# Optimization experiments

Hardware: AMD Instinct MI355X
Metric: run time of the kernel (lower is better)

## Reference

```python
import jax, jax.numpy as jnp
import numpy as np

M, N, T = 4, 48, 512
D_IN = M + N                 # GRU-net input dim (m+n)
H1 = D_IN * 10 * 8           # 4160
HID = M * M + N * N          # 2320 GRU hidden
H2 = M * N * 4               # 768
D_OUT = M * N                # 192


def setup_inputs() -> dict:
    key = jax.random.key(0)
    ks = jax.random.split(key, 12)
    s = lambda i, shape, sc=0.02: (jax.random.normal(ks[i], shape, jnp.float32) * sc)
    return {
        "A": jnp.eye(M, dtype=jnp.float32) + s(0, (M, M), 0.05),
        "C": s(1, (N, M + 1), 0.1),
        "x0": jax.random.normal(ks[2], (M,), jnp.float32),
        "h0": jax.random.normal(ks[3], (HID,), jnp.float32),  # randn init hidden (zero_hidden_state=False)
        "y_seq": jax.random.normal(ks[4], (N, T), jnp.float32),
        "W1": s(5, (H1, D_IN)), "b1": jnp.zeros((H1,), jnp.float32),
        "W_ih": s(6, (3 * HID, H1)), "W_hh": s(7, (3 * HID, HID)),
        "b_ih": jnp.zeros((3 * HID,), jnp.float32), "b_hh": jnp.zeros((3 * HID,), jnp.float32),
        "W2": s(8, (H2, HID)), "b2": jnp.zeros((H2,), jnp.float32),
        "W3": s(9, (D_OUT, H2)), "b3": jnp.zeros((D_OUT,), jnp.float32),
    }


def _l2norm(v):
    # torch F.normalize(p=2, eps=1e-12): v / max(||v||, eps)
    return v / jnp.maximum(jnp.linalg.norm(v), 1e-12)


def _gru_cell(x, h, W_ih, W_hh, b_ih, b_hh):
    gi = W_ih @ x + b_ih
    gh = W_hh @ h + b_hh
    i_r, i_z, i_n = jnp.split(gi, 3)
    h_r, h_z, h_n = jnp.split(gh, 3)
    r = jax.nn.sigmoid(i_r + h_r)
    z = jax.nn.sigmoid(i_z + h_z)
    n = jnp.tanh(i_n + r * h_n)
    return (1.0 - z) * n + z * h


def reference(A, C, x0, h0, y_seq, W1, b1, W_ih, W_hh, b_ih, b_hh, W2, b2, W3, b3):
    one = jnp.ones((1,), jnp.float32)

    def step(carry, y):
        x_prior, x_post, h = carry
        # step_prior (linear case)
        x_prev_prior = x_prior
        x_prior = A @ x_post
        m1y = C @ jnp.concatenate([x_prior, one])  # [N]
        # step_KGain_est: KGainNet_in = [norm(dy), norm(dx)]
        knet_in = jnp.concatenate([_l2norm(y - m1y), _l2norm(x_post - x_prev_prior)])
        l1 = jax.nn.relu(W1 @ knet_in + b1)
        h = _gru_cell(l1, h, W_ih, W_hh, b_ih, b_hh)
        l2 = jax.nn.relu(W2 @ h + b2)
        kg = ((W3 @ l2 + b3) / 10000.0).reshape(M, N)
        # KNet_step posterior update
        x_post = x_prior + kg @ (y - m1y)
        return (x_prior, x_post, h), x_post

    _, xs = jax.lax.scan(step, (x0, x0, h0), y_seq.T)  # scan over T
    return xs.T  # [M, T], matches forward_sequence output
```

## Files before the change

### kernel.cpp

```cpp
#include <hip/hip_runtime.h>
#include <stdint.h>
#include <stddef.h>

typedef float v2f __attribute__((ext_vector_type(2)));

#define HID   2320
#define G3    6960
#define KIH   4160
#define KHH   2320
#define NBLK  232
#define NL2B  192
#define NTHR  512
#define UPB   10
#define TSEQ  512
#define KRES  1600
#define INVWS (1.0f/128.0f)
#define SPINCAP (1u<<17)

#define WS_WIH8 0L
#define WS_W1E  28953600L
#define WS_HBP  29219840L
#define WS_SLT  29279232L
#define WS_END  29308928L

struct Offs {
  int l1s, hs, wih, whh, w2s, w3s, cs, as_, b3s, bih, bhh, b2s, gis, ghs,
      ts, inn, kn, dxs, xpri, xpo, b4, nrm, l2r, slp;
  int total;
};

__host__ __device__ inline Offs mkoffs(int res) {
  Offs o; int p = 0;
#define ALLOC(name, bytes) { p = (p + 15) & ~15; o.name = p; p += (bytes); }
  ALLOC(l1s, KIH*4) ALLOC(hs, HID*4)
  ALLOC(wih, res ? 30*KRES : 16) ALLOC(whh, res ? 30*KHH : 16)
  ALLOC(w2s, res ? 4*HID : 16)
  ALLOC(w3s, 16*48*4) ALLOC(cs, 240*4) ALLOC(as_, 64) ALLOC(b3s, 192*4)
  ALLOC(bih, 120) ALLOC(bhh, 120) ALLOC(b2s, 16)
  ALLOC(gis, 120) ALLOC(ghs, 120)
  ALLOC(ts, 64) ALLOC(inn, 192) ALLOC(kn, 256)
  ALLOC(dxs, 16) ALLOC(xpri, 16) ALLOC(xpo, 16) ALLOC(b4, 16) ALLOC(nrm, 16)
  ALLOC(l2r, 16) ALLOC(slp, 64)
#undef ALLOC
  o.total = (p + 63) & ~63;
  return o;
}

struct Params {
  const float *A, *C, *x0, *h0, *y, *W1, *b1, *Wih, *Whh, *bih, *bhh, *W2, *b2, *W3, *b3;
  const uint8_t *wih8, *w1e;
  uint64_t *hbp, *slt;
  float *out;
  int resident;
};

__device__ __forceinline__ uint8_t f2fp8(float v) {
  v = fminf(fmaxf(v * 128.f, -448.f), 448.f);
  int pk = __builtin_amdgcn_cvt_pk_fp8_f32(v, v, 0, false);
  return (uint8_t)(pk & 0xff);
}

__device__ __forceinline__ void pub64(uint64_t* a, uint32_t tag, float v) {
  uint64_t w = ((uint64_t)tag << 32) | (uint64_t)__float_as_uint(v);
  __hip_atomic_store(a, w, __ATOMIC_RELAXED, __HIP_MEMORY_SCOPE_AGENT);
}

template<int N>
__device__ __forceinline__ void poll_pkt(const uint64_t* base, uint32_t want,
                                         float* out, bool& dead) {
  uint64_t v[N];
  uint32_t spins = 0;
  for (;;) {
    bool ok = true;
#pragma unroll
    for (int k = 0; k < N; ++k)
      v[k] = __hip_atomic_load(base + k, __ATOMIC_RELAXED, __HIP_MEMORY_SCOPE_AGENT);
#pragma unroll
    for (int k = 0; k < N; ++k) ok &= ((uint32_t)(v[k] >> 32) == want);
    if (ok || dead) break;
    ++spins;
    if (spins > 8) __builtin_amdgcn_s_sleep(2);
    if (spins > SPINCAP) dead = true;
  }
#pragma unroll
  for (int k = 0; k < N; ++k) out[k] = __uint_as_float((uint32_t)v[k]);
}

__device__ __forceinline__ void dot8_lds(
    const float* __restrict__ acts, const uint8_t* __restrict__ w, int stride,
    int K, const int* lrows, int nr, int lane, float acc[4])
{
  int kb = 0;
  for (; kb + 256 <= K; kb += 256) {
    const float4 a = ((const float4*)(acts + kb))[lane];
#pragma unroll
    for (int j = 0; j < 4; ++j) if (j < nr) {
      uint32_t wb = *(const uint32_t*)(w + (size_t)lrows[j]*stride + kb + (lane<<2));
      v2f lo = __builtin_amdgcn_cvt_pk_f32_fp8((int)wb, false);
      v2f hi = __builtin_amdgcn_cvt_pk_f32_fp8((int)wb, true);
      acc[j] = fmaf(lo.x, a.x, acc[j]); acc[j] = fmaf(lo.y, a.y, acc[j]);
      acc[j] = fmaf(hi.x, a.z, acc[j]); acc[j] = fmaf(hi.y, a.w, acc[j]);
    }
  }
  int rem = K - kb;
  if ((lane << 2) < rem) {
    const float4 a = ((const float4*)(acts + kb))[lane];
#pragma unroll
    for (int j = 0; j < 4; ++j) if (j < nr) {
      uint32_t wb = *(const uint32_t*)(w + (size_t)lrows[j]*stride + kb + (lane<<2));
      v2f lo = __builtin_amdgcn_cvt_pk_f32_fp8((int)wb, false);
      v2f hi = __builtin_amdgcn_cvt_pk_f32_fp8((int)wb, true);
      acc[j] = fmaf(lo.x, a.x, acc[j]); acc[j] = fmaf(lo.y, a.y, acc[j]);
      acc[j] = fmaf(hi.x, a.z, acc[j]); acc[j] = fmaf(hi.y, a.w, acc[j]);
    }
  }
}

__device__ __forceinline__ void dot8_glb(
    const float* __restrict__ acts, const uint8_t* __restrict__ gw, int gstride,
    int K0, int K, const int* grows, int nr, int lane, float acc[4])
{
  int kb = K0;
  for (; kb + 512 <= K; kb += 512) {
    const float4 a0 = ((const float4*)(acts + kb))[lane*2];
    const float4 a1 = ((const float4*)(acts + kb))[lane*2 + 1];
#pragma unroll
    for (int j = 0; j < 4; ++j) if (j < nr) {
      uint2 wb = *(const uint2*)(gw + (size_t)grows[j]*gstride + kb + (lane<<3));
      v2f l0 = __builtin_amdgcn_cvt_pk_f32_fp8((int)wb.x, false);
      v2f h0 = __builtin_amdgcn_cvt_pk_f32_fp8((int)wb.x, true);
      v2f l1 = __builtin_amdgcn_cvt_pk_f32_fp8((int)wb.y, false);
      v2f h1 = __builtin_amdgcn_cvt_pk_f32_fp8((int)wb.y, true);
      acc[j] = fmaf(l0.x, a0.x, acc[j]); acc[j] = fmaf(l0.y, a0.y, acc[j]);
      acc[j] = fmaf(h0.x, a0.z, acc[j]); acc[j] = fmaf(h0.y, a0.w, acc[j]);
      acc[j] = fmaf(l1.x, a1.x, acc[j]); acc[j] = fmaf(l1.y, a1.y, acc[j]);
      acc[j] = fmaf(h1.x, a1.z, acc[j]); acc[j] = fmaf(h1.y, a1.w, acc[j]);
    }
  }
  for (int e = kb + lane; e < K; e += 64) {
    float a = acts[e];
#pragma unroll
    for (int j = 0; j < 4; ++j) if (j < nr) {
      v2f lo = __builtin_amdgcn_cvt_pk_f32_fp8(
          (int)(uint32_t)gw[(size_t)grows[j]*gstride + e], false);
      acc[j] = fmaf(lo.x, a, acc[j]);
    }
  }
}

__device__ __forceinline__ void dotf_glb(
    const float* __restrict__ acts, const float* __restrict__ gw, int gstride,
    int K, const int* grows, int nr, int lane, float acc[4])
{
  for (int k = lane; k < K; k += 64) {
    float a = acts[k];
#pragma unroll
    for (int j = 0; j < 4; ++j) if (j < nr)
      acc[j] = fmaf(gw[(size_t)grows[j]*gstride + k], a, acc[j]);
  }
}

extern "C" __global__ void __launch_bounds__(NTHR, 2) knet_main(Params p)
{
  extern __shared__ char smem[];
  const Offs o = mkoffs(p.resident);
  float*   L1S  = (float*)(smem + o.l1s);
  float*   HS   = (float*)(smem + o.hs);
  uint8_t* WIHR = (uint8_t*)(smem + o.wih);
  uint8_t* WHHR = (uint8_t*)(smem + o.whh);
  uint8_t* W2S  = (uint8_t*)(smem + o.w2s);
  float*   W3S  = (float*)(smem + o.w3s);
  float*   CS   = (float*)(smem + o.cs);
  float*   AS   = (float*)(smem + o.as_);
  float*   B3S  = (float*)(smem + o.b3s);
  float*   BIH  = (float*)(smem + o.bih);
  float*   BHH  = (float*)(smem + o.bhh);
  float*   B2S  = (float*)(smem + o.b2s);
  float*   GIS  = (float*)(smem + o.gis);
  float*   GHS  = (float*)(smem + o.ghs);
  float*   TS   = (float*)(smem + o.ts);
  float*   INNS = (float*)(smem + o.inn);
  float*   KN   = (float*)(smem + o.kn);
  float*   DXS  = (float*)(smem + o.dxs);
  float*   XPRI = (float*)(smem + o.xpri);
  float*   XPO  = (float*)(smem + o.xpo);
  float*   B4   = (float*)(smem + o.b4);
  float*   NRM  = (float*)(smem + o.nrm);
  float*   L2R  = (float*)(smem + o.l2r);
  float*   SLP  = (float*)(smem + o.slp);

  const int tid  = (int)threadIdx.x;
  const int bid  = (int)blockIdx.x;
  const int lane = tid & 63;
  const int wv   = tid >> 6;
  const int rows2 = (bid < NL2B) ? 4 : 0;
  const int r2s   = bid * 4;
  bool dead = false;

  int lrows[4] = {0,0,0,0}, grows[4] = {0,0,0,0};
  int nr = 0;
#pragma unroll
  for (int j = 0; j < 4; ++j) {
    int row = wv + 8*j;
    if (row < 30) { int u = row/3, g = row - 3*u;
      lrows[nr] = row; grows[nr] = g*HID + bid*UPB + u; ++nr; }
  }

  for (int i = tid; i < rows2*192; i += NTHR) { int rl = i/192, rem = i - rl*192;
    W3S[i] = p.W3[(size_t)rem*768 + (r2s + rl)]; }
  for (int i = tid; i < 240; i += NTHR) CS[i] = p.C[i];
  if (tid < 16) AS[tid] = p.A[tid];
  for (int i = tid; i < 192; i += NTHR) B3S[i] = p.b3[i];
  if (tid < rows2) B2S[tid] = p.b2[r2s + tid];
  if (tid < 30) {
    int u = tid/3, g = tid - 3*u, ug = bid*UPB + u;
    BIH[tid] = p.bih[g*HID + ug];
    BHH[tid] = p.bhh[g*HID + ug];
  }
  for (int i = tid; i < HID; i += NTHR) HS[i] = p.h0[i];
  if (p.resident) {
    const int kd = KRES >> 2;
    uint32_t* W32 = (uint32_t*)WIHR;
    for (int i = tid; i < 30*kd; i += NTHR) {
      int row = i / kd, c = i - row*kd;
      int u = row/3, g = row - 3*u, gr = g*HID + bid*UPB + u;
      W32[i] = ((const uint32_t*)p.wih8)[(size_t)gr*(KIH/4) + c];
    }
    for (int i = tid; i < 30*KHH; i += NTHR) {
      int row = i / KHH, k = i - row*KHH;
      int u = row/3, g = row - 3*u, gr = g*HID + bid*UPB + u;
      WHHR[i] = f2fp8(p.Whh[(size_t)gr*KHH + k]);
    }
    for (int i = tid; i < rows2*HID; i += NTHR) {
      int rl = i / HID, k = i - rl*HID;
      W2S[i] = f2fp8(p.W2[(size_t)(r2s+rl)*HID + k]);
    }
  }
  uint2 pf[4][5];
#pragma unroll
  for (int j = 0; j < 4; ++j)
#pragma unroll
    for (int i = 0; i < 5; ++i) pf[j][i] = make_uint2(0u, 0u);
#pragma unroll
  for (int j = 0; j < 4; ++j) if (j < nr)
#pragma unroll
    for (int i = 0; i < 5; ++i)
      pf[j][i] = *(const uint2*)(p.wih8 + (size_t)grows[j]*KIH + KRES + i*512 + (lane<<3));
  __syncthreads();

  auto small_chain = [&](int ycol) {
    if (tid < 48) {
      float s = CS[tid*5 + 4];
#pragma unroll
      for (int k = 0; k < 4; ++k) s += CS[tid*5 + k] * XPRI[k];
      INNS[tid] = p.y[(size_t)tid*TSEQ + ycol] - s;
    }
    __syncthreads();
    if (wv == 0) {
      float q = (lane < 48) ? INNS[lane]*INNS[lane] : 0.f;
#pragma unroll
      for (int m = 32; m >= 1; m >>= 1) q += __shfl_xor(q, m, 64);
      if (lane == 0) NRM[0] = fmaxf(sqrtf(q), 1e-12f);
    } else if (wv == 1) {
      float q = (lane < 4) ? DXS[lane]*DXS[lane] : 0.f;
#pragma unroll
      for (int m = 32; m >= 1; m >>= 1) q += __shfl_xor(q, m, 64);
      if (lane == 0) NRM[1] = fmaxf(sqrtf(q), 1e-12f);
    }
    __syncthreads();
    if (tid < 48) KN[tid] = INNS[tid] / NRM[0];
    else if (tid < 52) KN[tid] = DXS[tid-48] / NRM[1];
    else if (tid == 52) KN[tid] = 1.0f;
    else if (tid < 64) KN[tid] = 0.0f;
    else if (tid < 68) {
      int i = tid - 64; float s = 0;
      for (int j = 0; j < 48; ++j) s += B3S[i*48 + j] * INNS[j];
      B4[i] = s;
    }
    if (tid >= 128 && tid < 128 + rows2*4) {
      int idx = tid - 128, rl = idx >> 2, i = idx & 3;
      float s = 0;
      for (int j = 0; j < 48; ++j) s += W3S[rl*192 + i*48 + j] * INNS[j];
      TS[i*4 + rl] = s;
    }
    __syncthreads();
    {
      float4 kn[16];
#pragma unroll
      for (int c = 0; c < 16; ++c) kn[c] = ((const float4*)KN)[c];
      for (int r = tid; r < KIH; r += NTHR) {
        const uint4* wp = (const uint4*)(p.w1e + (size_t)r*64);
        float acc = 0.f;
#pragma unroll
        for (int q = 0; q < 4; ++q) {
          uint4 w = wp[q];
          v2f l0 = __builtin_amdgcn_cvt_pk_f32_fp8((int)w.x, false);
          v2f h0 = __builtin_amdgcn_cvt_pk_f32_fp8((int)w.x, true);
          v2f l1 = __builtin_amdgcn_cvt_pk_f32_fp8((int)w.y, false);
          v2f h1 = __builtin_amdgcn_cvt_pk_f32_fp8((int)w.y, true);
          v2f l2 = __builtin_amdgcn_cvt_pk_f32_fp8((int)w.z, false);
          v2f h2 = __builtin_amdgcn_cvt_pk_f32_fp8((int)w.z, true);
          v2f l3 = __builtin_amdgcn_cvt_pk_f32_fp8((int)w.w, false);
          v2f h3 = __builtin_amdgcn_cvt_pk_f32_fp8((int)w.w, true);
          float4 a0 = kn[q*4+0], a1 = kn[q*4+1], a2 = kn[q*4+2], a3 = kn[q*4+3];
          acc = fmaf(l0.x,a0.x,acc); acc = fmaf(l0.y,a0.y,acc);
          acc = fmaf(h0.x,a0.z,acc); acc = fmaf(h0.y,a0.w,acc);
          acc = fmaf(l1.x,a1.x,acc); acc = fmaf(l1.y,a1.y,acc);
          acc = fmaf(h1.x,a1.z,acc); acc = fmaf(h1.y,a1.w,acc);
          acc = fmaf(l2.x,a2.x,acc); acc = fmaf(l2.y,a2.y,acc);
          acc = fmaf(h2.x,a2.z,acc); acc = fmaf(h2.y,a2.w,acc);
          acc = fmaf(l3.x,a3.x,acc); acc = fmaf(l3.y,a3.y,acc);
          acc = fmaf(h3.x,a3.z,acc); acc = fmaf(h3.y,a3.w,acc);
        }
        L1S[r] = fmaxf(acc * INVWS, 0.f);
      }
    }
    __syncthreads();
  };

  auto ghh = [&]() {
    float acc[4] = {0,0,0,0};
    if (p.resident) dot8_lds(HS, WHHR, KHH, KHH, lrows, nr, lane, acc);
    else            dotf_glb(HS, p.Whh, KHH, KHH, grows, nr, lane, acc);
#pragma unroll
    for (int m = 32; m >= 1; m >>= 1)
#pragma unroll
      for (int j = 0; j < 4; ++j) acc[j] += __shfl_xor(acc[j], m, 64);
    if (lane == 0)
#pragma unroll
      for (int j = 0; j < 4; ++j) if (j < nr) GHS[lrows[j]] = acc[j];
  };

  if (tid < 4) { XPO[tid] = p.x0[tid]; DXS[tid] = 0.f; }
  __syncthreads();
  if (tid < 4) {
    float s = 0;
#pragma unroll
    for (int j = 0; j < 4; ++j) s += AS[tid*4 + j] * XPO[j];
    XPRI[tid] = s;
  }
  __syncthreads();
  small_chain(0);
  ghh();
  __syncthreads();

  for (int t = 0; t < TSEQ; ++t) {
    const int par = t & 1;
    const uint32_t want = (uint32_t)(t + 1);

    {
      float acc[4] = {0,0,0,0};
      if (p.resident) dot8_lds(L1S, WIHR, KRES, KRES, lrows, nr, lane, acc);
      else            dot8_glb(L1S, p.wih8, KIH, 0, KRES, grows, nr, lane, acc);
#pragma unroll
      for (int i = 0; i < 5; ++i) {
        const float4 a0 = ((const float4*)(L1S + KRES + i*512))[lane*2];
        const float4 a1 = ((const float4*)(L1S + KRES + i*512))[lane*2 + 1];
#pragma unroll
        for (int j = 0; j < 4; ++j) if (j < nr) {
          uint2 w = pf[j][i];
          v2f l0 = __builtin_amdgcn_cvt_pk_f32_fp8((int)w.x, false);
          v2f h0 = __builtin_amdgcn_cvt_pk_f32_fp8((int)w.x, true);
          v2f l1v = __builtin_amdgcn_cvt_pk_f32_fp8((int)w.y, false);
          v2f h1 = __builtin_amdgcn_cvt_pk_f32_fp8((int)w.y, true);
          acc[j] = fmaf(l0.x, a0.x, acc[j]); acc[j] = fmaf(l0.y, a0.y, acc[j]);
          acc[j] = fmaf(h0.x, a0.z, acc[j]); acc[j] = fmaf(h0.y, a0.w, acc[j]);
          acc[j] = fmaf(l1v.x, a1.x, acc[j]); acc[j] = fmaf(l1v.y, a1.y, acc[j]);
          acc[j] = fmaf(h1.x, a1.z, acc[j]); acc[j] = fmaf(h1.y, a1.w, acc[j]);
        }
      }
#pragma unroll
      for (int m = 32; m >= 1; m >>= 1)
#pragma unroll
        for (int j = 0; j < 4; ++j) acc[j] += __shfl_xor(acc[j], m, 64);
      if (lane == 0)
#pragma unroll
        for (int j = 0; j < 4; ++j) if (j < nr) GIS[lrows[j]] = acc[j];
    }
    __syncthreads();

    if (tid < UPB) {
      int ug = bid*UPB + tid, r0 = tid*3;
      float gi0 = GIS[r0+0]*INVWS + BIH[r0+0], gh0 = GHS[r0+0]*INVWS + BHH[r0+0];
      float gi1 = GIS[r0+1]*INVWS + BIH[r0+1], gh1 = GHS[r0+1]*INVWS + BHH[r0+1];
      float gi2 = GIS[r0+2]*INVWS + BIH[r0+2], gh2 = GHS[r0+2]*INVWS + BHH[r0+2];
      float rg = 1.f/(1.f + expf(-(gi0+gh0)));
      float zg = 1.f/(1.f + expf(-(gi1+gh1)));
      float ng = tanhf(gi2 + rg*gh2);
      float hnew = (1.f - zg)*ng + zg*HS[ug];
      pub64(p.hbp + (((size_t)par*NBLK + bid) << 4) + tid, want, hnew);
    }
    __syncthreads();

    if (wv < 4) {
      int idx = (wv << 6) | lane;
      if (idx < NBLK) {
        float v[10];
        poll_pkt<10>(p.hbp + (((size_t)par*NBLK + idx) << 4), want, v, dead);
#pragma unroll
        for (int k = 0; k < 10; ++k) HS[idx*10 + k] = v[k];
      }
    }
    __syncthreads();

    if (rows2 && wv >= 4) {
      const int rl = wv - 4;
      float a2 = 0.f;
      if (p.resident) {
        int kb = 0;
        for (; kb + 256 <= HID; kb += 256) {
          const float4 a = ((const float4*)(HS + kb))[lane];
          uint32_t wb = *(const uint32_t*)(W2S + rl*HID + kb + (lane<<2));
          v2f lo = __builtin_amdgcn_cvt_pk_f32_fp8((int)wb, false);
          v2f hi = __builtin_amdgcn_cvt_pk_f32_fp8((int)wb, true);
          a2 = fmaf(lo.x, a.x, a2); a2 = fmaf(lo.y, a.y, a2);
          a2 = fmaf(hi.x, a.z, a2); a2 = fmaf(hi.y, a.w, a2);
        }
        if ((lane << 2) < HID - kb) {
          const float4 a = ((const float4*)(HS + kb))[lane];
          uint32_t wb = *(const uint32_t*)(W2S + rl*HID + kb + (lane<<2));
          v2f lo = __builtin_amdgcn_cvt_pk_f32_fp8((int)wb, false);
          v2f hi = __builtin_amdgcn_cvt_pk_f32_fp8((int)wb, true);
          a2 = fmaf(lo.x, a.x, a2); a2 = fmaf(lo.y, a.y, a2);
          a2 = fmaf(hi.x, a.z, a2); a2 = fmaf(hi.y, a.w, a2);
        }
        a2 *= INVWS;
      } else {
        for (int k = lane; k < HID; k += 64)
          a2 = fmaf(p.W2[(size_t)(r2s+rl)*HID + k], HS[k], a2);
      }
#pragma unroll
      for (int m = 32; m >= 1; m >>= 1) a2 += __shfl_xor(a2, m, 64);
      if (lane == 0) L2R[rl] = fmaxf(a2 + B2S[rl], 0.f);
    }
    __syncthreads();
    if (rows2 && tid < 4) {
      float cp = L2R[0]*TS[tid*4+0] + L2R[1]*TS[tid*4+1]
               + L2R[2]*TS[tid*4+2] + L2R[3]*TS[tid*4+3];
      pub64(p.slt + (((size_t)par*NBLK + bid) << 3) + tid, want, cp);
    }

    ghh();

    if (wv < 3) {
      int idx = (wv << 6) | lane;
      float v[4];
      poll_pkt<4>(p.slt + (((size_t)par*NBLK + idx) << 3), want, v, dead);
      float s0 = v[0], s1 = v[1], s2 = v[2], s3 = v[3];
#pragma unroll
      for (int m = 32; m >= 1; m >>= 1) {
        s0 += __shfl_xor(s0, m, 64); s1 += __shfl_xor(s1, m, 64);
        s2 += __shfl_xor(s2, m, 64); s3 += __shfl_xor(s3, m, 64);
      }
      if (lane == 0) {
        SLP[wv*4+0] = s0; SLP[wv*4+1] = s1; SLP[wv*4+2] = s2; SLP[wv*4+3] = s3;
      }
    }
    __syncthreads();

    if (tid < 4) {
      float c = SLP[tid] + SLP[4 + tid] + SLP[8 + tid];
      float xp = XPRI[tid] + (c + B4[tid]) * 1e-4f;
      XPO[tid] = xp;
      if (bid == 0) p.out[(size_t)tid*TSEQ + t] = xp;
    }
    __syncthreads();
    if (t + 1 < TSEQ) {
      if (tid < 4) {
        float xo = XPO[tid];
        DXS[tid] = xo - XPRI[tid];
        float s = 0;
#pragma unroll
        for (int j = 0; j < 4; ++j) s += AS[tid*4 + j] * XPO[j];
        XPRI[tid] = s;
      }
      __syncthreads();
      small_chain(t + 1);
    }
  }
}

extern "C" __global__ void knet_cvt_fp8(const float* __restrict__ src,
                                        uint8_t* __restrict__ dst, long n4) {
  long stride = (long)gridDim.x * blockDim.x;
  for (long i = (long)blockIdx.x*blockDim.x + threadIdx.x; i < n4; i += stride) {
    float4 v = ((const float4*)src)[i];
    float a0 = fminf(fmaxf(v.x * 128.f, -448.f), 448.f);
    float a1 = fminf(fmaxf(v.y * 128.f, -448.f), 448.f);
    float a2 = fminf(fmaxf(v.z * 128.f, -448.f), 448.f);
    float a3 = fminf(fmaxf(v.w * 128.f, -448.f), 448.f);
    int pk = __builtin_amdgcn_cvt_pk_fp8_f32(a0, a1, 0, false);
    pk = __builtin_amdgcn_cvt_pk_fp8_f32(a2, a3, pk, true);
    ((uint32_t*)dst)[i] = (uint32_t)pk;
  }
}

extern "C" __global__ void knet_build_w1e(const float* __restrict__ W1,
                                          const float* __restrict__ b1,
                                          uint8_t* __restrict__ dst) {
  int r = blockIdx.x * blockDim.x + threadIdx.x;
  if (r >= KIH) return;
  float v[64];
#pragma unroll 13
  for (int q = 0; q < 13; ++q) {
    float4 w = ((const float4*)(W1 + (size_t)r*52))[q];
    v[q*4+0] = w.x; v[q*4+1] = w.y; v[q*4+2] = w.z; v[q*4+3] = w.w;
  }
  v[52] = b1[r];
  for (int i = 53; i < 64; ++i) v[i] = 0.f;
  uint32_t out[16];
#pragma unroll 16
  for (int d = 0; d < 16; ++d) {
    float a0 = fminf(fmaxf(v[d*4+0] * 128.f, -448.f), 448.f);
    float a1 = fminf(fmaxf(v[d*4+1] * 128.f, -448.f), 448.f);
    float a2 = fminf(fmaxf(v[d*4+2] * 128.f, -448.f), 448.f);
    float a3 = fminf(fmaxf(v[d*4+3] * 128.f, -448.f), 448.f);
    int pk = __builtin_amdgcn_cvt_pk_fp8_f32(a0, a1, 0, false);
    pk = __builtin_amdgcn_cvt_pk_fp8_f32(a2, a3, pk, true);
    out[d] = (uint32_t)pk;
  }
  uint4* dp = (uint4*)(dst + (size_t)r*64);
#pragma unroll 4
  for (int q = 0; q < 4; ++q)
    dp[q] = make_uint4(out[q*4+0], out[q*4+1], out[q*4+2], out[q*4+3]);
}

extern "C" void kernel_launch(void* const* d_in, const int* in_sizes, int n_in,
                              void* d_out, int out_size, void* d_ws, size_t ws_size,
                              hipStream_t stream)
{
  if (ws_size < (size_t)WS_END) return;
  uint8_t* ws = (uint8_t*)d_ws;

  knet_cvt_fp8<<<2048, 256, 0, stream>>>((const float*)d_in[7], ws + WS_WIH8,
                                         (long)G3*KIH/4);
  knet_build_w1e<<<(KIH + 255)/256, 256, 0, stream>>>(
      (const float*)d_in[5], (const float*)d_in[6], ws + WS_W1E);

  int resident = 1;
  Offs o = mkoffs(resident);
  hipError_t e = hipFuncSetAttribute((const void*)knet_main,
                                     hipFuncAttributeMaxDynamicSharedMemorySize,
                                     o.total);
  if (e != hipSuccess) {
    resident = 0; o = mkoffs(resident);
    (void)hipFuncSetAttribute((const void*)knet_main,
                              hipFuncAttributeMaxDynamicSharedMemorySize, o.total);
  }

  Params p;
  p.A   = (const float*)d_in[0];  p.C   = (const float*)d_in[1];
  p.x0  = (const float*)d_in[2];  p.h0  = (const float*)d_in[3];
  p.y   = (const float*)d_in[4];
  p.W1  = (const float*)d_in[5];  p.b1  = (const float*)d_in[6];
  p.Wih = (const float*)d_in[7];  p.Whh = (const float*)d_in[8];
  p.bih = (const float*)d_in[9];  p.bhh = (const float*)d_in[10];
  p.W2  = (const float*)d_in[11]; p.b2  = (const float*)d_in[12];
  p.W3  = (const float*)d_in[13]; p.b3  = (const float*)d_in[14];
  p.wih8 = ws + WS_WIH8;
  p.w1e  = ws + WS_W1E;
  p.hbp  = (uint64_t*)(ws + WS_HBP);
  p.slt  = (uint64_t*)(ws + WS_SLT);
  p.out  = (float*)d_out;
  p.resident = resident;

  knet_main<<<NBLK, NTHR, (size_t)o.total, stream>>>(p);
}
```

Measured before the change: 8.289 ms.

## Collapse per-step small-chain into a single wavefront and drop block barriers

The per-timestep Kalman bookkeeping (posterior update, prior, innovation, norms, KN vector, B4/TS projections) now runs in wave 0 using register shuffles instead of several block-wide phases separated by __syncthreads. The GRU hidden value owned by each thread stays in a register, which removes one barrier after the hidden update. Fewer block barriers per step on the serial critical path is the intended saving. The cost is more serial work packed onto one wave, and the change relies on wave-level ordering (wave_barrier) for the LDS INNS reads.

```diff
diff --git a/kernel.cpp b/kernel.cpp
--- a/kernel.cpp
+++ b/kernel.cpp
@@ -84,6 +84,27 @@
   }
 #pragma unroll
   for (int k = 0; k < N; ++k) out[k] = __uint_as_float((uint32_t)v[k]);
+}
+
+__device__ __forceinline__ float fma16(uint4 w, float4 a0, float4 a1,
+                                       float4 a2, float4 a3, float acc) {
+  v2f l0 = __builtin_amdgcn_cvt_pk_f32_fp8((int)w.x, false);
+  v2f h0 = __builtin_amdgcn_cvt_pk_f32_fp8((int)w.x, true);
+  v2f l1 = __builtin_amdgcn_cvt_pk_f32_fp8((int)w.y, false);
+  v2f h1 = __builtin_amdgcn_cvt_pk_f32_fp8((int)w.y, true);
+  v2f l2 = __builtin_amdgcn_cvt_pk_f32_fp8((int)w.z, false);
+  v2f h2 = __builtin_amdgcn_cvt_pk_f32_fp8((int)w.z, true);
+  v2f l3 = __builtin_amdgcn_cvt_pk_f32_fp8((int)w.w, false);
+  v2f h3 = __builtin_amdgcn_cvt_pk_f32_fp8((int)w.w, true);
+  acc = fmaf(l0.x,a0.x,acc); acc = fmaf(l0.y,a0.y,acc);
+  acc = fmaf(h0.x,a0.z,acc); acc = fmaf(h0.y,a0.w,acc);
+  acc = fmaf(l1.x,a1.x,acc); acc = fmaf(l1.y,a1.y,acc);
+  acc = fmaf(h1.x,a1.z,acc); acc = fmaf(h1.y,a1.w,acc);
+  acc = fmaf(l2.x,a2.x,acc); acc = fmaf(l2.y,a2.y,acc);
+  acc = fmaf(h2.x,a2.z,acc); acc = fmaf(h2.y,a2.w,acc);
+  acc = fmaf(l3.x,a3.x,acc); acc = fmaf(l3.y,a3.y,acc);
+  acc = fmaf(h3.x,a3.z,acc); acc = fmaf(h3.y,a3.w,acc);
+  return acc;
 }
 
 __device__ __forceinline__ void dot8_lds(
@@ -218,6 +239,7 @@
     BHH[tid] = p.bhh[g*HID + ug];
   }
   for (int i = tid; i < HID; i += NTHR) HS[i] = p.h0[i];
+  float myh = (tid < UPB) ? p.h0[(size_t)bid*UPB + tid] : 0.f;
   if (p.resident) {
     const int kd = KRES >> 2;
     uint32_t* W32 = (uint32_t*)WIHR;
@@ -248,74 +270,20 @@
       pf[j][i] = *(const uint2*)(p.wih8 + (size_t)grows[j]*KIH + KRES + i*512 + (lane<<3));
   __syncthreads();
 
-  auto small_chain = [&](int ycol) {
-    if (tid < 48) {
-      float s = CS[tid*5 + 4];
-#pragma unroll
-      for (int k = 0; k < 4; ++k) s += CS[tid*5 + k] * XPRI[k];
-      INNS[tid] = p.y[(size_t)tid*TSEQ + ycol] - s;
-    }
-    __syncthreads();
-    if (wv == 0) {
-      float q = (lane < 48) ? INNS[lane]*INNS[lane] : 0.f;
-#pragma unroll
-      for (int m = 32; m >= 1; m >>= 1) q += __shfl_xor(q, m, 64);
-      if (lane == 0) NRM[0] = fmaxf(sqrtf(q), 1e-12f);
-    } else if (wv == 1) {
-      float q = (lane < 4) ? DXS[lane]*DXS[lane] : 0.f;
-#pragma unroll
-      for (int m = 32; m >= 1; m >>= 1) q += __shfl_xor(q, m, 64);
-      if (lane == 0) NRM[1] = fmaxf(sqrtf(q), 1e-12f);
-    }
-    __syncthreads();
-    if (tid < 48) KN[tid] = INNS[tid] / NRM[0];
-    else if (tid < 52) KN[tid] = DXS[tid-48] / NRM[1];
-    else if (tid == 52) KN[tid] = 1.0f;
-    else if (tid < 64) KN[tid] = 0.0f;
-    else if (tid < 68) {
-      int i = tid - 64; float s = 0;
-      for (int j = 0; j < 48; ++j) s += B3S[i*48 + j] * INNS[j];
-      B4[i] = s;
-    }
-    if (tid >= 128 && tid < 128 + rows2*4) {
-      int idx = tid - 128, rl = idx >> 2, i = idx & 3;
-      float s = 0;
-      for (int j = 0; j < 48; ++j) s += W3S[rl*192 + i*48 + j] * INNS[j];
-      TS[i*4 + rl] = s;
-    }
-    __syncthreads();
-    {
-      float4 kn[16];
-#pragma unroll
-      for (int c = 0; c < 16; ++c) kn[c] = ((const float4*)KN)[c];
-      for (int r = tid; r < KIH; r += NTHR) {
-        const uint4* wp = (const uint4*)(p.w1e + (size_t)r*64);
-        float acc = 0.f;
-#pragma unroll
-        for (int q = 0; q < 4; ++q) {
-          uint4 w = wp[q];
-          v2f l0 = __builtin_amdgcn_cvt_pk_f32_fp8((int)w.x, false);
-          v2f h0 = __builtin_amdgcn_cvt_pk_f32_fp8((int)w.x, true);
-          v2f l1 = __builtin_amdgcn_cvt_pk_f32_fp8((int)w.y, false);
-          v2f h1 = __builtin_amdgcn_cvt_pk_f32_fp8((int)w.y, true);
-          v2f l2 = __builtin_amdgcn_cvt_pk_f32_fp8((int)w.z, false);
-          v2f h2 = __builtin_amdgcn_cvt_pk_f32_fp8((int)w.z, true);
-          v2f l3 = __builtin_amdgcn_cvt_pk_f32_fp8((int)w.w, false);
-          v2f h3 = __builtin_amdgcn_cvt_pk_f32_fp8((int)w.w, true);
-          float4 a0 = kn[q*4+0], a1 = kn[q*4+1], a2 = kn[q*4+2], a3 = kn[q*4+3];
-          acc = fmaf(l0.x,a0.x,acc); acc = fmaf(l0.y,a0.y,acc);
-          acc = fmaf(h0.x,a0.z,acc); acc = fmaf(h0.y,a0.w,acc);
-          acc = fmaf(l1.x,a1.x,acc); acc = fmaf(l1.y,a1.y,acc);
-          acc = fmaf(h1.x,a1.z,acc); acc = fmaf(h1.y,a1.w,acc);
-          acc = fmaf(l2.x,a2.x,acc); acc = fmaf(l2.y,a2.y,acc);
-          acc = fmaf(h2.x,a2.z,acc); acc = fmaf(h2.y,a2.w,acc);
-          acc = fmaf(l3.x,a3.x,acc); acc = fmaf(l3.y,a3.y,acc);
-          acc = fmaf(h3.x,a3.z,acc); acc = fmaf(h3.y,a3.w,acc);
-        }
-        L1S[r] = fmaxf(acc * INVWS, 0.f);
-      }
-    }
-    __syncthreads();
+  auto full_l1 = [&]() {
+    float4 kn[16];
+#pragma unroll
+    for (int c = 0; c < 16; ++c) kn[c] = ((const float4*)KN)[c];
+    for (int r = tid; r < KIH; r += NTHR) {
+      const uint4* wp = (const uint4*)(p.w1e + (size_t)r*64);
+      float acc = 0.f;
+#pragma unroll
+      for (int q = 0; q < 4; ++q) {
+        uint4 w = wp[q];
+        acc = fma16(w, kn[q*4+0], kn[q*4+1], kn[q*4+2], kn[q*4+3], acc);
+      }
+      L1S[r] = fmaxf(acc * INVWS, 0.f);
+    }
   };
 
   auto ghh = [&]() {
@@ -340,9 +308,46 @@
     XPRI[tid] = s;
   }
   __syncthreads();
-  small_chain(0);
+  if (tid < 48) {
+    float s = CS[tid*5 + 4];
+#pragma unroll
+    for (int k = 0; k < 4; ++k) s += CS[tid*5 + k] * XPRI[k];
+    INNS[tid] = p.y[(size_t)tid*TSEQ + 0] - s;
+  }
+  __syncthreads();
+  if (wv == 0) {
+    float q = (lane < 48) ? INNS[lane]*INNS[lane] : 0.f;
+#pragma unroll
+    for (int m = 32; m >= 1; m >>= 1) q += __shfl_xor(q, m, 64);
+    if (lane == 0) NRM[0] = fmaxf(sqrtf(q), 1e-12f);
+  } else if (wv == 1) {
+    float q = (lane < 4) ? DXS[lane]*DXS[lane] : 0.f;
+#pragma unroll
+    for (int m = 32; m >= 1; m >>= 1) q += __shfl_xor(q, m, 64);
+    if (lane == 0) NRM[1] = fmaxf(sqrtf(q), 1e-12f);
+  }
+  __syncthreads();
+  if (tid < 48) KN[tid] = INNS[tid] / NRM[0];
+  else if (tid < 52) KN[tid] = DXS[tid-48] / NRM[1];
+  else if (tid == 52) KN[tid] = 1.0f;
+  else if (tid < 64) KN[tid] = 0.0f;
+  else if (tid < 68) {
+    int i = tid - 64; float s = 0;
+    for (int j = 0; j < 48; ++j) s += B3S[i*48 + j] * INNS[j];
+    B4[i] = s;
+  }
+  if (rows2 && tid >= 128 && tid < 144) {
+    int idx = tid - 128, rl = idx >> 2, i = idx & 3;
+    float s = 0;
+    for (int j = 0; j < 48; ++j) s += W3S[rl*192 + i*48 + j] * INNS[j];
+    TS[i*4 + rl] = s;
+  }
+  __syncthreads();
+  full_l1();
   ghh();
   __syncthreads();
+  float myXpri = 0.f, myB4 = 0.f;
+  if (wv == 0 && lane < 4) { myXpri = XPRI[lane]; myB4 = B4[lane]; }
 
   for (int t = 0; t < TSEQ; ++t) {
     const int par = t & 1;
@@ -380,17 +385,17 @@
     __syncthreads();
 
     if (tid < UPB) {
-      int ug = bid*UPB + tid, r0 = tid*3;
+      int r0 = tid*3;
       float gi0 = GIS[r0+0]*INVWS + BIH[r0+0], gh0 = GHS[r0+0]*INVWS + BHH[r0+0];
       float gi1 = GIS[r0+1]*INVWS + BIH[r0+1], gh1 = GHS[r0+1]*INVWS + BHH[r0+1];
       float gi2 = GIS[r0+2]*INVWS + BIH[r0+2], gh2 = GHS[r0+2]*INVWS + BHH[r0+2];
       float rg = 1.f/(1.f + expf(-(gi0+gh0)));
       float zg = 1.f/(1.f + expf(-(gi1+gh1)));
       float ng = tanhf(gi2 + rg*gh2);
-      float hnew = (1.f - zg)*ng + zg*HS[ug];
+      float hnew = (1.f - zg)*ng + zg*myh;
+      myh = hnew;
       pub64(p.hbp + (((size_t)par*NBLK + bid) << 4) + tid, want, hnew);
     }
-    __syncthreads();
 
     if (wv < 4) {
       int idx = (wv << 6) | lane;
@@ -458,24 +463,64 @@
     }
     __syncthreads();
 
-    if (tid < 4) {
-      float c = SLP[tid] + SLP[4 + tid] + SLP[8 + tid];
-      float xp = XPRI[tid] + (c + B4[tid]) * 1e-4f;
-      XPO[tid] = xp;
-      if (bid == 0) p.out[(size_t)tid*TSEQ + t] = xp;
+    if (wv == 0) {
+      float xp = 0.f, dx = 0.f;
+      if (lane < 4) {
+        float c = SLP[lane] + SLP[4 + lane] + SLP[8 + lane];
+        xp = myXpri + (c + myB4) * 1e-4f;
+        if (bid == 0) p.out[(size_t)lane*TSEQ + t] = xp;
+        dx = xp - myXpri;
+      }
+      if (t + 1 < TSEQ) {
+        float xp0 = __shfl(xp, 0), xp1 = __shfl(xp, 1),
+              xp2 = __shfl(xp, 2), xp3 = __shfl(xp, 3);
+        float xpri_new = 0.f;
+        if (lane < 4)
+          xpri_new = AS[lane*4+0]*xp0 + AS[lane*4+1]*xp1
+                   + AS[lane*4+2]*xp2 + AS[lane*4+3]*xp3;
+        if (lane < 4) myXpri = xpri_new;
+        float xr0 = __shfl(xpri_new, 0), xr1 = __shfl(xpri_new, 1),
+              xr2 = __shfl(xpri_new, 2), xr3 = __shfl(xpri_new, 3);
+        float qd = dx * dx;
+#pragma unroll
+        for (int m = 32; m >= 1; m >>= 1) qd += __shfl_xor(qd, m, 64);
+        float n1 = fmaxf(sqrtf(qd), 1e-12f);
+        float inn = 0.f;
+        if (lane < 48) {
+          float s = CS[lane*5 + 4] + CS[lane*5+0]*xr0 + CS[lane*5+1]*xr1
+                  + CS[lane*5+2]*xr2 + CS[lane*5+3]*xr3;
+          inn = p.y[(size_t)lane*TSEQ + (t+1)] - s;
+          INNS[lane] = inn;
+        }
+        float qi = inn * inn;
+#pragma unroll
+        for (int m = 32; m >= 1; m >>= 1) qi += __shfl_xor(qi, m, 64);
+        float n0 = fmaxf(sqrtf(qi), 1e-12f);
+        float knv;
+        if (lane < 48)        knv = inn / n0;
+        else if (lane < 52)   knv = __shfl(dx, lane - 48) / n1;
+        else if (lane == 52)  knv = 1.0f;
+        else                  knv = 0.0f;
+        KN[lane] = knv;
+        __builtin_amdgcn_wave_barrier();
+        if (lane < 4) {
+          float s = 0.f;
+          for (int j = 0; j < 48; ++j) s += B3S[lane*48 + j] * INNS[j];
+          myB4 = s;
+        }
+        if (rows2 && lane >= 8 && lane < 24) {
+          int idx = lane - 8, rl = idx >> 2, i = idx & 3;
+          float s = 0.f;
+          for (int j = 0; j < 48; ++j) s += W3S[rl*192 + i*48 + j] * INNS[j];
+          TS[i*4 + rl] = s;
+        }
+      }
     }
     __syncthreads();
+
     if (t + 1 < TSEQ) {
-      if (tid < 4) {
-        float xo = XPO[tid];
-        DXS[tid] = xo - XPRI[tid];
-        float s = 0;
-#pragma unroll
-        for (int j = 0; j < 4; ++j) s += AS[tid*4 + j] * XPO[j];
-        XPRI[tid] = s;
-      }
+      full_l1();
       __syncthreads();
-      small_chain(t + 1);
     }
   }
 }
```

Result: slower. 10.42 ms (+25.7%).
